# Kernel optimization log

Hardware: AMD Instinct MI355X
Metric: run time of the kernel (lower is better)

The kernel has to match this reference:

```python
import jax, jax.numpy as jnp
import numpy as np

G, N, F_IN, H, C = 128, 512, 128, 128, 10
LAMB = 1.0
NEG_SLOPE = 0.2
P_EDGE = 32.0 / N  # avg degree ~32


def setup_inputs() -> dict:
    key = jax.random.key(0)
    ks = jax.random.split(key, 12)
    x = jax.random.normal(ks[0], (G, N, F_IN), dtype=jnp.float32)
    # symmetric 0/1 adjacency without self loops (per-graph dense block)
    a = (jax.random.uniform(ks[1], (G, N, N)) < P_EDGE).astype(jnp.float32)
    adj = jnp.maximum(a, jnp.swapaxes(a, 1, 2)) * (1.0 - jnp.eye(N, dtype=jnp.float32))

    def lin(k, fi, fo):
        return (jax.random.normal(k, (fi, fo), dtype=jnp.float32) / np.float32(np.sqrt(fi)))

    return {
        "x": x, "adj": adj,
        "W1": lin(ks[2], F_IN, H), "b1": jnp.zeros((H,), jnp.float32),
        "W2": lin(ks[3], H, H), "b2": jnp.zeros((H,), jnp.float32),
        "W3": lin(ks[4], H, H), "b3": jnp.zeros((H,), jnp.float32),
        "att1_s": 0.1 * jax.random.normal(ks[5], (H,), dtype=jnp.float32),
        "att1_d": 0.1 * jax.random.normal(ks[6], (H,), dtype=jnp.float32),
        "att2_s": 0.1 * jax.random.normal(ks[7], (H,), dtype=jnp.float32),
        "att2_d": 0.1 * jax.random.normal(ks[8], (H,), dtype=jnp.float32),
        "Wl1": lin(ks[9], 2 * H, H), "bl1": jnp.zeros((H,), jnp.float32),
        "Wl2": lin(ks[10], H, H // 2), "bl2": jnp.zeros((H // 2,), jnp.float32),
        "Wl3": lin(ks[11], H // 2, C), "bl3": jnp.zeros((C,), jnp.float32),
    }


def gcn(x, adj, W, b):
    # GCNConv: D^{-1/2} (A + I) D^{-1/2} X W + b  (self-loop weight 1, edge weights in adj)
    deg = adj.sum(-1) + 1.0                              # [G, n]
    dinv = jax.lax.rsqrt(deg)
    xw = x @ W                                           # [G, n, H]
    agg = jnp.einsum('gij,gjf->gif', adj, dinv[..., None] * xw)
    return dinv[..., None] * agg + (dinv * dinv)[..., None] * xw + b


def info_score(x, adj):
    # HGP-SL node information score: row-wise L1 norm of (I - D^{-1} A) X
    deg = jnp.maximum(adj.sum(-1), 1.0)
    agg = jnp.einsum('gij,gjf->gif', adj, x) / deg[..., None]
    return jnp.sum(jnp.abs(x - agg), axis=-1)            # [G, n]


def hgpsl_pool(x, adj, att_s, att_d, k):
    # top-k node selection by information score, then structure learning:
    # dense (sample=False) path: e_ij = leaky_relu(att.[x_i||x_j]) + lamb*A_ij, softmax over j
    s = info_score(x, adj)
    _, idx = jax.lax.top_k(s, k)                         # [G, k]
    xk = jnp.take_along_axis(x, idx[..., None], axis=1)  # [G, k, H]
    g = jnp.arange(x.shape[0])[:, None, None]
    ak = adj[g, idx[:, :, None], idx[:, None, :]]        # induced adjacency [G, k, k]
    e = jax.nn.leaky_relu((xk @ att_s)[:, :, None] + (xk @ att_d)[:, None, :], NEG_SLOPE)
    attn = jax.nn.softmax(e + LAMB * ak, axis=-1)        # new learned edge weights
    return xk, attn


def readout(x):
    # gmp || gap over nodes
    return jnp.concatenate([x.max(axis=1), x.mean(axis=1)], axis=-1)


def reference(x, adj, W1, b1, W2, b2, W3, b3, att1_s, att1_d, att2_s, att2_d,
              Wl1, bl1, Wl2, bl2, Wl3, bl3):
    h = jax.nn.relu(gcn(x, adj, W1, b1))
    h, a1 = hgpsl_pool(h, adj, att1_s, att1_d, N // 2)
    x1 = readout(h)
    h = jax.nn.relu(gcn(h, a1, W2, b2))
    h, a2 = hgpsl_pool(h, a1, att2_s, att2_d, N // 4)
    x2 = readout(h)
    h = jax.nn.relu(gcn(h, a2, W3, b3))
    x3 = readout(h)
    z = jax.nn.relu(x1) + jax.nn.relu(x2) + jax.nn.relu(x3)
    z = jax.nn.relu(z @ Wl1 + bl1)
    z = jax.nn.relu(z @ Wl2 + bl2)
    return jax.nn.softmax(z @ Wl3 + bl3, axis=-1)
```

## Files before the change

### kernel.cpp

```cpp
#include <hip/hip_runtime.h>

#define Gg   128
#define N1   512
#define FH   128
#define K1   256
#define K2   128

typedef __bf16 bf16x8 __attribute__((ext_vector_type(8)));
typedef float  floatx4 __attribute__((ext_vector_type(4)));

__device__ inline float wredsum(float v) {
#pragma unroll
    for (int o = 32; o; o >>= 1) v += __shfl_xor(v, o, 64);
    return v;
}
__device__ inline float wredmax(float v) {
#pragma unroll
    for (int o = 32; o; o >>= 1) v = fmaxf(v, __shfl_xor(v, o, 64));
    return v;
}
__device__ inline unsigned short bf_rne(float x) {
    unsigned u = __float_as_uint(x);
    return (unsigned short)((u + 0x7fffu + ((u >> 16) & 1u)) >> 16);
}
__device__ __forceinline__ void gll16(const void* gsrc, void* lds) {
    __builtin_amdgcn_global_load_lds(
        (const __attribute__((address_space(1))) unsigned int*)gsrc,
        (__attribute__((address_space(3))) unsigned int*)lds, 16, 0, 0);
}

__global__ __launch_bounds__(256) void k_prep_gemm(const float* __restrict__ adj,
        unsigned short* __restrict__ adjbf,
        float* __restrict__ dinv_gcn, float* __restrict__ dinv_info,
        const float* __restrict__ A, const float* __restrict__ W, float* __restrict__ C) {
    __shared__ float Al[64][68];
    __shared__ float Wl[64][132];
    if (blockIdx.x < Gg * N1 / 64) {
        long long row0 = (long long)blockIdx.x * 64;
        int tid = threadIdx.x, tr = tid >> 4, tc = tid & 15;
        float acc[4][8] = {};
        for (int ch = 0; ch < 2; ++ch) {
            for (int p = tid; p < 1024; p += 256) {
                int r = p >> 4, c4 = p & 15;
                *(float4*)&Al[r][c4 * 4] = *(const float4*)(A + (row0 + r) * 128 + ch * 64 + c4 * 4);
            }
            for (int p = tid; p < 2048; p += 256) {
                int r = p >> 5, c4 = p & 31;
                *(float4*)&Wl[r][c4 * 4] = *(const float4*)(W + (ch * 64 + r) * 128 + c4 * 4);
            }
            __syncthreads();
            for (int k = 0; k < 64; ++k) {
                float4 w0 = *(const float4*)&Wl[k][tc * 8];
                float4 w1 = *(const float4*)&Wl[k][tc * 8 + 4];
                float w[8] = {w0.x, w0.y, w0.z, w0.w, w1.x, w1.y, w1.z, w1.w};
#pragma unroll
                for (int i = 0; i < 4; ++i) {
                    float a = Al[tr * 4 + i][k];
#pragma unroll
                    for (int j = 0; j < 8; ++j) acc[i][j] = fmaf(a, w[j], acc[i][j]);
                }
            }
            __syncthreads();
        }
#pragma unroll
        for (int i = 0; i < 4; ++i) {
            long long r = row0 + tr * 4 + i;
            *(float4*)(C + r * 128 + tc * 8)     = make_float4(acc[i][0], acc[i][1], acc[i][2], acc[i][3]);
            *(float4*)(C + r * 128 + tc * 8 + 4) = make_float4(acc[i][4], acc[i][5], acc[i][6], acc[i][7]);
        }
    } else {
        int wave = threadIdx.x >> 6, lane = threadIdx.x & 63;
        long long row = (long long)(blockIdx.x - Gg * N1 / 64) * 4 + wave;
        const float* ar = adj + row * N1;
        float s = 0.f;
        unsigned short ub[8] __attribute__((aligned(16)));
#pragma unroll
        for (int c = 0; c < 2; ++c) {
            float4 v = *(const float4*)(ar + lane * 8 + c * 4);
            s += (v.x + v.y) + (v.z + v.w);
            ub[c * 4 + 0] = (unsigned short)(__float_as_uint(v.x) >> 16);
            ub[c * 4 + 1] = (unsigned short)(__float_as_uint(v.y) >> 16);
            ub[c * 4 + 2] = (unsigned short)(__float_as_uint(v.z) >> 16);
            ub[c * 4 + 3] = (unsigned short)(__float_as_uint(v.w) >> 16);
        }
        *(uint4*)(adjbf + row * N1 + lane * 8) = *(const uint4*)ub;
        s = wredsum(s);
        if (lane == 0) {
            dinv_gcn[row]  = rsqrtf(s + 1.0f);
            dinv_info[row] = 1.0f / fmaxf(s, 1.0f);
        }
    }
}

__global__ __launch_bounds__(256) void k_tsplit(const float* __restrict__ feat,
        const float* __restrict__ rs,
        unsigned short* __restrict__ Thi, unsigned short* __restrict__ Tmid,
        unsigned short* __restrict__ Tlo) {
    __shared__ float tile[64 * 65];
    int b = blockIdx.x;
    int g = b >> 4, rb = (b >> 1) & 7, cb = b & 1;
    int t = threadIdx.x;
    {
        int r0 = t >> 4, c4 = t & 15;
#pragma unroll
        for (int i = 0; i < 4; ++i) {
            int r = r0 + i * 16;
            float4 v = *(const float4*)(feat + ((long long)g * 512 + rb * 64 + r) * 128 + cb * 64 + c4 * 4);
            if (rs) {
                float sc = rs[(long long)g * 512 + rb * 64 + r];
                v.x *= sc; v.y *= sc; v.z *= sc; v.w *= sc;
            }
            tile[r * 65 + c4 * 4 + 0] = v.x;
            tile[r * 65 + c4 * 4 + 1] = v.y;
            tile[r * 65 + c4 * 4 + 2] = v.z;
            tile[r * 65 + c4 * 4 + 3] = v.w;
        }
    }
    __syncthreads();
    int tf = t >> 2, chunk = t & 3;
    unsigned short hbuf[16] __attribute__((aligned(16)));
    unsigned short mbuf[16] __attribute__((aligned(16)));
    unsigned short lbuf[16] __attribute__((aligned(16)));
#pragma unroll
    for (int i = 0; i < 16; ++i) {
        int m = chunk * 16 + i;
        float v = tile[m * 65 + tf];
        unsigned short h = bf_rne(v);
        float fh = __uint_as_float((unsigned)h << 16);
        float r1 = v - fh;
        unsigned short md = bf_rne(r1);
        float fm = __uint_as_float((unsigned)md << 16);
        float r2 = r1 - fm;
        unsigned short lo = bf_rne(r2);
        hbuf[i] = h; mbuf[i] = md; lbuf[i] = lo;
    }
    int sxz = (tf >> 1) & 3;
    int c0 = (chunk & 1) * 2;
    int p0 = (c0 ^ sxz) * 8, p1 = ((c0 + 1) ^ sxz) * 8;
    long long obase = (long long)g * 65536 + (rb * 2 + (chunk >> 1)) * 4096
                    + (cb * 64 + tf) * 32;
    *(uint4*)(Thi + obase + p0)  = *(const uint4*)&hbuf[0];
    *(uint4*)(Thi + obase + p1)  = *(const uint4*)&hbuf[8];
    *(uint4*)(Tmid + obase + p0) = *(const uint4*)&mbuf[0];
    *(uint4*)(Tmid + obase + p1) = *(const uint4*)&mbuf[8];
    *(uint4*)(Tlo + obase + p0)  = *(const uint4*)&lbuf[0];
    *(uint4*)(Tlo + obase + p1)  = *(const uint4*)&lbuf[8];
}

template<int EPI>
__global__ __launch_bounds__(256) void k_aggmm(const unsigned short* __restrict__ adjbf,
        const unsigned short* __restrict__ Bhi, const unsigned short* __restrict__ Bmid,
        const unsigned short* __restrict__ Blo,
        const float* __restrict__ dvec, const float* __restrict__ hx,
        const float* __restrict__ bias, float* __restrict__ outH, float* __restrict__ outS) {
    __shared__ unsigned short Al[2][4096];
    __shared__ unsigned short Blin[2][3][4096];
    __shared__ float sred[2][128];
    int b = blockIdx.x;
    int g  = (b & 7) + ((b >> 5) << 3);
    int rb = (b >> 3) & 3;
    int tid = threadIdx.x;
    int w = tid >> 6, lane = tid & 63;
    int wm = w >> 1, wn = w & 1;
    int ln = lane & 15, quad = lane >> 4;
    int aoff = ((quad ^ ((lane >> 1) & 3)) << 4);
    floatx4 acc[4][4];
#pragma unroll
    for (int i = 0; i < 4; ++i)
#pragma unroll
        for (int j = 0; j < 4; ++j) { floatx4 z = {0.f, 0.f, 0.f, 0.f}; acc[i][j] = z; }

    const char* bsrc0 = (const char*)(Bhi  + (long long)g * 65536);
    const char* bsrc1 = (const char*)(Bmid + (long long)g * 65536);
    const char* bsrc2 = (const char*)(Blo  + (long long)g * 65536);
    int r1 = w * 32 + (lane >> 2);
    int c1 = (lane & 3) ^ ((r1 >> 1) & 3);
    int r2 = r1 + 16;
    int c2 = (lane & 3) ^ ((r2 >> 1) & 3);
    const unsigned short* abase = adjbf + ((long long)g * 512 + rb * 128) * 512;
    const unsigned short* asrc1 = abase + (long long)r1 * 512 + c1 * 8;
    const unsigned short* asrc2 = abase + (long long)r2 * 512 + c2 * 8;

#define STAGE(bi, kkv) do {                                                   \
        char* aldst = (char*)&Al[bi][0] + w * 2048;                           \
        gll16(asrc1 + (kkv), aldst);                                          \
        gll16(asrc2 + (kkv), aldst + 1024);                                   \
        long long soff = (long long)((kkv) >> 5) * 8192 + (w * 2048) + (lane << 4); \
        char* l0 = (char*)&Blin[bi][0][0] + w * 2048;                         \
        char* l1 = (char*)&Blin[bi][1][0] + w * 2048;                         \
        char* l2 = (char*)&Blin[bi][2][0] + w * 2048;                         \
        gll16(bsrc0 + soff,        l0);                                       \
        gll16(bsrc0 + soff + 1024, l0 + 1024);                                \
        gll16(bsrc1 + soff,        l1);                                       \
        gll16(bsrc1 + soff + 1024, l1 + 1024);                                \
        gll16(bsrc2 + soff,        l2);                                       \
        gll16(bsrc2 + soff + 1024, l2 + 1024);                                \
    } while (0)

    STAGE(0, 0);
    for (int kk = 0; kk < 512; kk += 32) {
        int cur = (kk >> 5) & 1;
        if (kk + 32 < 512) {
            STAGE(cur ^ 1, kk + 32);
            asm volatile("s_waitcnt vmcnt(8)" ::: "memory");
        } else {
            asm volatile("s_waitcnt vmcnt(0)" ::: "memory");
        }
        __builtin_amdgcn_sched_barrier(0);
        __builtin_amdgcn_s_barrier();
        bf16x8 af[4];
#pragma unroll
        for (int tm = 0; tm < 4; ++tm)
            af[tm] = *(const bf16x8*)((const char*)&Al[cur][0] + (wm * 64 + tm * 16 + ln) * 64 + aoff);
#pragma unroll
        for (int s = 0; s < 3; ++s) {
#pragma unroll
            for (int tn = 0; tn < 4; ++tn) {
                bf16x8 bfr = *(const bf16x8*)((const char*)&Blin[cur][s][0]
                                              + (wn * 64 + tn * 16 + ln) * 64 + aoff);
#pragma unroll
                for (int tm = 0; tm < 4; ++tm)
                    acc[tm][tn] = __builtin_amdgcn_mfma_f32_16x16x32_bf16(af[tm], bfr, acc[tm][tn], 0, 0, 0);
            }
        }
        __builtin_amdgcn_sched_barrier(0);
        __builtin_amdgcn_s_barrier();
    }
#undef STAGE
    long long rowbase = (long long)g * 512 + rb * 128;
    if (EPI == 0) {
#pragma unroll
        for (int tm = 0; tm < 4; ++tm)
#pragma unroll
        for (int r = 0; r < 4; ++r) {
            int ml = wm * 64 + tm * 16 + quad * 4 + r;
            long long grow = rowbase + ml;
            float di = dvec[grow];
#pragma unroll
            for (int tn = 0; tn < 4; ++tn) {
                int nc = wn * 64 + tn * 16 + ln;
                float hv = hx[grow * 128 + nc];
                float o = fmaxf(fmaf(di, acc[tm][tn][r] + di * hv, bias[nc]), 0.f);
                outH[grow * 128 + nc] = o;
            }
        }
    } else {
#pragma unroll
        for (int tm = 0; tm < 4; ++tm)
#pragma unroll
        for (int r = 0; r < 4; ++r) {
            int ml = wm * 64 + tm * 16 + quad * 4 + r;
            long long grow = rowbase + ml;
            float di = dvec[grow];
            float v = 0.f;
#pragma unroll
            for (int tn = 0; tn < 4; ++tn) {
                int nc = wn * 64 + tn * 16 + ln;
                float hv = hx[grow * 128 + nc];
                v += fabsf(hv - acc[tm][tn][r] * di);
            }
            v += __shfl_xor(v, 1); v += __shfl_xor(v, 2);
            v += __shfl_xor(v, 4); v += __shfl_xor(v, 8);
            if (ln == 0) sred[wn][ml] = v;
        }
        __syncthreads();
        if (tid < 128) outS[rowbase + tid] = sred[0][tid] + sred[1][tid];
    }
}

__global__ __launch_bounds__(256) void k_gemm_rw(const float* __restrict__ A,
        const float* __restrict__ W, float* __restrict__ C,
        const float* __restrict__ rs) {
    __shared__ float Al[64][68];
    __shared__ float Wl[64][132];
    long long row0 = (long long)blockIdx.x * 64;
    int tid = threadIdx.x, tr = tid >> 4, tc = tid & 15;
    float acc[4][8] = {};
    for (int ch = 0; ch < 2; ++ch) {
        for (int p = tid; p < 1024; p += 256) {
            int r = p >> 4, c4 = p & 15;
            *(float4*)&Al[r][c4 * 4] = *(const float4*)(A + (row0 + r) * 128 + ch * 64 + c4 * 4);
        }
        for (int p = tid; p < 2048; p += 256) {
            int r = p >> 5, c4 = p & 31;
            *(float4*)&Wl[r][c4 * 4] = *(const float4*)(W + (ch * 64 + r) * 128 + c4 * 4);
        }
        __syncthreads();
        for (int k = 0; k < 64; ++k) {
            float4 w0 = *(const float4*)&Wl[k][tc * 8];
            float4 w1 = *(const float4*)&Wl[k][tc * 8 + 4];
            float w[8] = {w0.x, w0.y, w0.z, w0.w, w1.x, w1.y, w1.z, w1.w};
#pragma unroll
            for (int i = 0; i < 4; ++i) {
                float a = Al[tr * 4 + i][k];
#pragma unroll
                for (int j = 0; j < 8; ++j) acc[i][j] = fmaf(a, w[j], acc[i][j]);
            }
        }
        __syncthreads();
    }
#pragma unroll
    for (int i = 0; i < 4; ++i) {
        long long r = row0 + tr * 4 + i;
        float sc = rs ? rs[r] : 1.0f;
        *(float4*)(C + r * 128 + tc * 8)     = make_float4(sc * acc[i][0], sc * acc[i][1], sc * acc[i][2], sc * acc[i][3]);
        *(float4*)(C + r * 128 + tc * 8 + 4) = make_float4(sc * acc[i][4], sc * acc[i][5], sc * acc[i][6], sc * acc[i][7]);
    }
}

template<int NT, int KSEL>
__global__ __launch_bounds__(256) void k_topk(const float* __restrict__ s, int* __restrict__ idx) {
    __shared__ unsigned long long keys[NT];
    int g = blockIdx.x;
    const float* sg = s + g * NT;
    for (int t = threadIdx.x; t < NT; t += 256) {
        unsigned int b = __float_as_uint(sg[t]);
        unsigned int ord = (b & 0x80000000u) ? ~b : (b | 0x80000000u);
        keys[t] = ((unsigned long long)(~ord) << 32) | (unsigned int)t;
    }
    __syncthreads();
    for (int k = 2; k <= NT; k <<= 1) {
        for (int j = k >> 1; j > 0; j >>= 1) {
            for (int i = threadIdx.x; i < NT; i += 256) {
                int l = i ^ j;
                if (l > i) {
                    bool dir = ((i & k) == 0);
                    unsigned long long a = keys[i], b2 = keys[l];
                    bool sw = dir ? (a > b2) : (a < b2);
                    if (sw) { keys[i] = b2; keys[l] = a; }
                }
            }
            __syncthreads();
        }
    }
    for (int t = threadIdx.x; t < KSEL; t += 256)
        idx[g * KSEL + t] = (int)(keys[t] & 0xffffffffu);
}

template<int KK>
__global__ __launch_bounds__(256) void k_gather(const float* __restrict__ h, int srcN,
        const int* __restrict__ idx, const float* __restrict__ atts, const float* __restrict__ attd,
        float* __restrict__ xk, float* __restrict__ as_, float* __restrict__ ad_) {
    int wave = threadIdx.x >> 6, lane = threadIdx.x & 63;
    int r = blockIdx.x * 4 + wave;
    int g = r / KK;
    int j = idx[r];
    float2 v = *(const float2*)(h + ((long long)g * srcN + j) * 128 + lane * 2);
    *(float2*)(xk + (long long)r * 128 + lane * 2) = v;
    float2 sv = *(const float2*)(atts + lane * 2);
    float2 dv = *(const float2*)(attd + lane * 2);
    float ps = v.x * sv.x + v.y * sv.y;
    float pd = v.x * dv.x + v.y * dv.y;
    ps = wredsum(ps); pd = wredsum(pd);
    if (lane == 0) { as_[r] = ps; ad_[r] = pd; }
}

template<int KK, int SRCN, bool BF16>
__global__ __launch_bounds__(256) void k_attnro(const void* __restrict__ adjSrc,
        const int* __restrict__ idx, const float* __restrict__ as_, const float* __restrict__ ad_,
        float* __restrict__ attn, float* __restrict__ dgo, float* __restrict__ dio,
        const float* __restrict__ xk, float* __restrict__ xo) {
    constexpr int E = KK / 64;
    constexpr int nAttn = Gg * KK / 4;
    __shared__ int   idxL[KK];
    __shared__ float adL[KK];
    __shared__ float rowL[4][SRCN];
    if ((int)blockIdx.x >= nAttn) {
        int g = blockIdx.x - nAttn, t = threadIdx.x;
        if (t < 128) {
            const float* p = xk + (long long)g * KK * 128 + t;
            float m = -1e30f, s = 0.f;
            for (int r = 0; r < KK; ++r) { float v = p[r * 128]; m = fmaxf(m, v); s += v; }
            xo[g * 256 + t] = m;
            xo[g * 256 + 128 + t] = s * (1.0f / KK);
        }
        return;
    }
    int bpg = KK / 4;
    int g = blockIdx.x / bpg;
    int wave = threadIdx.x >> 6, lane = threadIdx.x & 63;
    int i = (blockIdx.x % bpg) * 4 + wave;
    for (int t = threadIdx.x; t < KK; t += 256) { idxL[t] = idx[g * KK + t]; adL[t] = ad_[g * KK + t]; }
    __syncthreads();
    int ri = idxL[i];
    if (BF16) {
        const unsigned short* arow = (const unsigned short*)adjSrc + ((long long)g * SRCN + ri) * SRCN;
        for (int c = lane; c < SRCN; c += 64)
            rowL[wave][c] = __uint_as_float((unsigned)arow[c] << 16);
    } else {
        const float* arow = (const float*)adjSrc + ((long long)g * SRCN + ri) * SRCN;
        for (int c = lane; c < SRCN; c += 64) rowL[wave][c] = arow[c];
    }
    float asi = as_[g * KK + i];
    float vals[E];
    float m = -1e30f;
#pragma unroll
    for (int e = 0; e < E; ++e) {
        int j = e * 64 + lane;
        float x = asi + adL[j];
        x = (x >= 0.f) ? x : 0.2f * x;
        x += rowL[wave][idxL[j]];
        vals[e] = x; m = fmaxf(m, x);
    }
    m = wredmax(m);
    float S = 0.f;
#pragma unroll
    for (int e = 0; e < E; ++e) { vals[e] = expf(vals[e] - m); S += vals[e]; }
    S = wredsum(S);
    float inv = 1.f / S, rs = 0.f;
    float* orow = attn + ((long long)g * KK + i) * KK;
#pragma unroll
    for (int e = 0; e < E; ++e) { float p = vals[e] * inv; rs += p; orow[e * 64 + lane] = p; }
    rs = wredsum(rs);
    if (lane == 0) { dgo[g * KK + i] = rsqrtf(rs + 1.f); dio[g * KK + i] = 1.f / fmaxf(rs, 1.f); }
}

template<int KK, bool SCALEY, int EPI>
__global__ __launch_bounds__(256) void k_agg(const float* __restrict__ A, const float* __restrict__ Y,
        const float* __restrict__ dg, const float* __restrict__ di_,
        const float* __restrict__ bias, const float* __restrict__ hx,
        float* __restrict__ outH, float* __restrict__ outS) {
    __shared__ float Al[64][68];
    __shared__ float Yl[64][132];
    __shared__ float red[64][17];
    constexpr int RB = KK / 64;
    int g = blockIdx.x / RB;
    int rb = blockIdx.x % RB;
    const float* Ag = A + (long long)g * KK * KK;
    const float* Yg = Y + (long long)g * KK * 128;
    int tid = threadIdx.x, tr = tid >> 4, tc = tid & 15;
    float acc[4][8] = {};
    for (int ch = 0; ch < KK / 64; ++ch) {
        for (int p = tid; p < 1024; p += 256) {
            int r = p >> 4, c4 = p & 15;
            *(float4*)&Al[r][c4 * 4] = *(const float4*)(Ag + (rb * 64 + r) * KK + ch * 64 + c4 * 4);
        }
        for (int p = tid; p < 2048; p += 256) {
            int r = p >> 5, c4 = p & 31;
            float4 v = *(const float4*)(Yg + (ch * 64 + r) * 128 + c4 * 4);
            if (SCALEY) { float sc = dg[g * KK + ch * 64 + r]; v.x *= sc; v.y *= sc; v.z *= sc; v.w *= sc; }
            *(float4*)&Yl[r][c4 * 4] = v;
        }
        __syncthreads();
        for (int k = 0; k < 64; ++k) {
            float4 w0 = *(const float4*)&Yl[k][tc * 8];
            float4 w1 = *(const float4*)&Yl[k][tc * 8 + 4];
            float w[8] = {w0.x, w0.y, w0.z, w0.w, w1.x, w1.y, w1.z, w1.w};
#pragma unroll
            for (int i = 0; i < 4; ++i) {
                float a = Al[tr * 4 + i][k];
#pragma unroll
                for (int j = 0; j < 8; ++j) acc[i][j] = fmaf(a, w[j], acc[i][j]);
            }
        }
        __syncthreads();
    }
    int i0 = rb * 64 + tr * 4;
    if (EPI == 0) {
#pragma unroll
        for (int i = 0; i < 4; ++i) {
            long long gi = (long long)g * KK + i0 + i;
            float d = dg[gi], dd = d * d;
            float4 x0 = *(const float4*)(hx + gi * 128 + tc * 8);
            float4 x1 = *(const float4*)(hx + gi * 128 + tc * 8 + 4);
            float4 b0 = *(const float4*)(bias + tc * 8);
            float4 b1 = *(const float4*)(bias + tc * 8 + 4);
            float4 o0, o1;
            o0.x = fmaxf(fmaf(d, acc[i][0], fmaf(dd, x0.x, b0.x)), 0.f);
            o0.y = fmaxf(fmaf(d, acc[i][1], fmaf(dd, x0.y, b0.y)), 0.f);
            o0.z = fmaxf(fmaf(d, acc[i][2], fmaf(dd, x0.z, b0.z)), 0.f);
            o0.w = fmaxf(fmaf(d, acc[i][3], fmaf(dd, x0.w, b0.w)), 0.f);
            o1.x = fmaxf(fmaf(d, acc[i][4], fmaf(dd, x1.x, b1.x)), 0.f);
            o1.y = fmaxf(fmaf(d, acc[i][5], fmaf(dd, x1.y, b1.y)), 0.f);
            o1.z = fmaxf(fmaf(d, acc[i][6], fmaf(dd, x1.z, b1.z)), 0.f);
            o1.w = fmaxf(fmaf(d, acc[i][7], fmaf(dd, x1.w, b1.w)), 0.f);
            *(float4*)(outH + gi * 128 + tc * 8)     = o0;
            *(float4*)(outH + gi * 128 + tc * 8 + 4) = o1;
        }
    } else {
#pragma unroll
        for (int i = 0; i < 4; ++i) {
            long long gi = (long long)g * KK + i0 + i;
            float d = di_[gi];
            float4 x0 = *(const float4*)(hx + gi * 128 + tc * 8);
            float4 x1 = *(const float4*)(hx + gi * 128 + tc * 8 + 4);
            float p = fabsf(x0.x - acc[i][0] * d) + fabsf(x0.y - acc[i][1] * d)
                    + fabsf(x0.z - acc[i][2] * d) + fabsf(x0.w - acc[i][3] * d)
                    + fabsf(x1.x - acc[i][4] * d) + fabsf(x1.y - acc[i][5] * d)
                    + fabsf(x1.z - acc[i][6] * d) + fabsf(x1.w - acc[i][7] * d);
            red[tr * 4 + i][tc] = p;
        }
        __syncthreads();
        if (tid < 64) {
            float s = 0.f;
#pragma unroll
            for (int t = 0; t < 16; ++t) s += red[tid][t];
            outS[(long long)g * KK + rb * 64 + tid] = s;
        }
    }
}

__global__ __launch_bounds__(128) void k_mlp(const float* __restrict__ x1, const float* __restrict__ x2,
        const float* __restrict__ h3,
        const float* __restrict__ Wl1, const float* __restrict__ bl1,
        const float* __restrict__ Wl2, const float* __restrict__ bl2,
        const float* __restrict__ Wl3, const float* __restrict__ bl3,
        float* __restrict__ out) {
    __shared__ float z[256], z1[128], z2[64], lg[10];
    int g = blockIdx.x, t = threadIdx.x;
    {
        const float* p = h3 + (long long)g * K2 * 128 + t;
        float m = -1e30f, s = 0.f;
        for (int r = 0; r < K2; ++r) { float v = p[r * 128]; m = fmaxf(m, v); s += v; }
        float x3a = m, x3b = s * (1.0f / K2);
        z[t]       = fmaxf(x1[g * 256 + t], 0.f)       + fmaxf(x2[g * 256 + t], 0.f)       + fmaxf(x3a, 0.f);
        z[t + 128] = fmaxf(x1[g * 256 + 128 + t], 0.f) + fmaxf(x2[g * 256 + 128 + t], 0.f) + fmaxf(x3b, 0.f);
    }
    __syncthreads();
    {
        float acc = bl1[t];
        for (int k = 0; k < 256; ++k) acc = fmaf(z[k], Wl1[k * 128 + t], acc);
        z1[t] = fmaxf(acc, 0.f);
    }
    __syncthreads();
    if (t < 64) {
        float acc = bl2[t];
        for (int k = 0; k < 128; ++k) acc = fmaf(z1[k], Wl2[k * 64 + t], acc);
        z2[t] = fmaxf(acc, 0.f);
    }
    __syncthreads();
    if (t < 10) {
        float acc = bl3[t];
        for (int k = 0; k < 64; ++k) acc = fmaf(z2[k], Wl3[k * 10 + t], acc);
        lg[t] = acc;
    }
    __syncthreads();
    if (t == 0) {
        float m = -1e30f;
        for (int c = 0; c < 10; ++c) m = fmaxf(m, lg[c]);
        float S = 0.f;
        float e[10];
        for (int c = 0; c < 10; ++c) { e[c] = expf(lg[c] - m); S += e[c]; }
        float inv = 1.f / S;
        for (int c = 0; c < 10; ++c) out[g * 10 + c] = e[c] * inv;
    }
}

extern "C" void kernel_launch(void* const* d_in, const int* in_sizes, int n_in,
                              void* d_out, int out_size, void* d_ws, size_t ws_size,
                              hipStream_t stream) {
    const float* x     = (const float*)d_in[0];
    const float* adj   = (const float*)d_in[1];
    const float* W1    = (const float*)d_in[2];
    const float* b1    = (const float*)d_in[3];
    const float* W2    = (const float*)d_in[4];
    const float* b2    = (const float*)d_in[5];
    const float* W3    = (const float*)d_in[6];
    const float* b3    = (const float*)d_in[7];
    const float* att1s = (const float*)d_in[8];
    const float* att1d = (const float*)d_in[9];
    const float* att2s = (const float*)d_in[10];
    const float* att2d = (const float*)d_in[11];
    const float* Wl1   = (const float*)d_in[12];
    const float* bl1   = (const float*)d_in[13];
    const float* Wl2   = (const float*)d_in[14];
    const float* bl2   = (const float*)d_in[15];
    const float* Wl3   = (const float*)d_in[16];
    const float* bl3   = (const float*)d_in[17];
    float* out = (float*)d_out;

    char* ws = (char*)d_ws;
    unsigned short* Thi  = (unsigned short*)(ws + 0);
    unsigned short* Tmid = (unsigned short*)(ws + 16777216);
    unsigned short* Tlo  = (unsigned short*)(ws + 33554432);
    float* xk1 = (float*)(ws + 0);
    float* xw2 = (float*)(ws + 16777216);
    float* h2  = (float*)(ws + 33554432);
    float* xk2 = (float*)(ws + 16777216);
    float* a2  = (float*)(ws + 25165824);
    float* xw3 = (float*)(ws + 0);
    float* h3  = (float*)(ws + 8388608);
    float* dxw1 = (float*)(ws + 50331648);
    float* h1   = dxw1;
    float* a1   = dxw1;
    float* s1      = (float*)(ws + 83886080);
    int*   idx1    = (int*)  (ws + 84148224);
    float* as1     = (float*)(ws + 84279296);
    float* ad1     = (float*)(ws + 84410368);
    float* dinv_g1 = (float*)(ws + 84541440);
    float* dinv_i1 = (float*)(ws + 84803584);
    float* dinv_g2 = (float*)(ws + 85065728);
    float* dinv_i2 = (float*)(ws + 85196800);
    float* x1r     = (float*)(ws + 85327872);
    float* s2      = (float*)(ws + 85458944);
    int*   idx2    = (int*)  (ws + 85590016);
    float* as2     = (float*)(ws + 85655552);
    float* ad2     = (float*)(ws + 85721088);
    float* dinv_g3 = (float*)(ws + 85786624);
    float* dinv_i3 = (float*)(ws + 85852160);
    float* x2r     = (float*)(ws + 85917696);
    unsigned short* adjbf = (unsigned short*)(ws + 100663296);

    k_prep_gemm<<<Gg * N1 / 64 + Gg * N1 / 4, 256, 0, stream>>>(adj, adjbf, dinv_g1, dinv_i1, x, W1, dxw1);
    k_tsplit<<<Gg * 16, 256, 0, stream>>>(dxw1, dinv_g1, Thi, Tmid, Tlo);
    k_aggmm<0><<<Gg * 4, 256, 0, stream>>>(adjbf, Thi, Tmid, Tlo, dinv_g1, dxw1, b1, h1, nullptr);
    k_tsplit<<<Gg * 16, 256, 0, stream>>>(h1, nullptr, Thi, Tmid, Tlo);
    k_aggmm<1><<<Gg * 4, 256, 0, stream>>>(adjbf, Thi, Tmid, Tlo, dinv_i1, h1, nullptr, nullptr, s1);
    k_topk<N1, K1><<<Gg, 256, 0, stream>>>(s1, idx1);
    k_gather<K1><<<Gg * K1 / 4, 256, 0, stream>>>(h1, N1, idx1, att1s, att1d, xk1, as1, ad1);
    k_attnro<K1, N1, true><<<Gg * K1 / 4 + Gg, 256, 0, stream>>>(adjbf, idx1, as1, ad1, a1, dinv_g2, dinv_i2, xk1, x1r);

    k_gemm_rw<<<Gg * K1 / 64, 256, 0, stream>>>(xk1, W2, xw2, nullptr);
    k_agg<K1, true, 0><<<Gg * (K1 / 64), 256, 0, stream>>>(a1, xw2, dinv_g2, dinv_i2, b2, xw2, h2, nullptr);
    k_agg<K1, false, 1><<<Gg * (K1 / 64), 256, 0, stream>>>(a1, h2, dinv_g2, dinv_i2, b2, h2, nullptr, s2);
    k_topk<K1, K2><<<Gg, 256, 0, stream>>>(s2, idx2);
    k_gather<K2><<<Gg * K2 / 4, 256, 0, stream>>>(h2, K1, idx2, att2s, att2d, xk2, as2, ad2);
    k_attnro<K2, K1, false><<<Gg * K2 / 4 + Gg, 256, 0, stream>>>(a1, idx2, as2, ad2, a2, dinv_g3, dinv_i3, xk2, x2r);

    k_gemm_rw<<<Gg * K2 / 64, 256, 0, stream>>>(xk2, W3, xw3, nullptr);
    k_agg<K2, true, 0><<<Gg * (K2 / 64), 256, 0, stream>>>(a2, xw3, dinv_g3, dinv_i3, b3, xw3, h3, nullptr);

    k_mlp<<<Gg, 128, 0, stream>>>(x1r, x2r, h3, Wl1, bl1, Wl2, bl2, Wl3, bl3, out);
}
```

Before: 580.4 us.

## Reorder first GCN layer to aggregate inputs before applying W1 via split-bf16 MFMA

```diff
diff --git a/kernel.cpp b/kernel.cpp
--- a/kernel.cpp
+++ b/kernel.cpp
@@ -29,75 +29,57 @@
         (__attribute__((address_space(3))) unsigned int*)lds, 16, 0, 0);
 }
 
-__global__ __launch_bounds__(256) void k_prep_gemm(const float* __restrict__ adj,
+__global__ __launch_bounds__(256) void k_prep(const float* __restrict__ adj,
         unsigned short* __restrict__ adjbf,
-        float* __restrict__ dinv_gcn, float* __restrict__ dinv_info,
-        const float* __restrict__ A, const float* __restrict__ W, float* __restrict__ C) {
-    __shared__ float Al[64][68];
-    __shared__ float Wl[64][132];
-    if (blockIdx.x < Gg * N1 / 64) {
-        long long row0 = (long long)blockIdx.x * 64;
-        int tid = threadIdx.x, tr = tid >> 4, tc = tid & 15;
-        float acc[4][8] = {};
-        for (int ch = 0; ch < 2; ++ch) {
-            for (int p = tid; p < 1024; p += 256) {
-                int r = p >> 4, c4 = p & 15;
-                *(float4*)&Al[r][c4 * 4] = *(const float4*)(A + (row0 + r) * 128 + ch * 64 + c4 * 4);
-            }
-            for (int p = tid; p < 2048; p += 256) {
-                int r = p >> 5, c4 = p & 31;
-                *(float4*)&Wl[r][c4 * 4] = *(const float4*)(W + (ch * 64 + r) * 128 + c4 * 4);
-            }
-            __syncthreads();
-            for (int k = 0; k < 64; ++k) {
-                float4 w0 = *(const float4*)&Wl[k][tc * 8];
-                float4 w1 = *(const float4*)&Wl[k][tc * 8 + 4];
-                float w[8] = {w0.x, w0.y, w0.z, w0.w, w1.x, w1.y, w1.z, w1.w};
-#pragma unroll
-                for (int i = 0; i < 4; ++i) {
-                    float a = Al[tr * 4 + i][k];
-#pragma unroll
-                    for (int j = 0; j < 8; ++j) acc[i][j] = fmaf(a, w[j], acc[i][j]);
-                }
-            }
-            __syncthreads();
-        }
-#pragma unroll
-        for (int i = 0; i < 4; ++i) {
-            long long r = row0 + tr * 4 + i;
-            *(float4*)(C + r * 128 + tc * 8)     = make_float4(acc[i][0], acc[i][1], acc[i][2], acc[i][3]);
-            *(float4*)(C + r * 128 + tc * 8 + 4) = make_float4(acc[i][4], acc[i][5], acc[i][6], acc[i][7]);
-        }
-    } else {
-        int wave = threadIdx.x >> 6, lane = threadIdx.x & 63;
-        long long row = (long long)(blockIdx.x - Gg * N1 / 64) * 4 + wave;
-        const float* ar = adj + row * N1;
-        float s = 0.f;
-        unsigned short ub[8] __attribute__((aligned(16)));
-#pragma unroll
-        for (int c = 0; c < 2; ++c) {
-            float4 v = *(const float4*)(ar + lane * 8 + c * 4);
-            s += (v.x + v.y) + (v.z + v.w);
-            ub[c * 4 + 0] = (unsigned short)(__float_as_uint(v.x) >> 16);
-            ub[c * 4 + 1] = (unsigned short)(__float_as_uint(v.y) >> 16);
-            ub[c * 4 + 2] = (unsigned short)(__float_as_uint(v.z) >> 16);
-            ub[c * 4 + 3] = (unsigned short)(__float_as_uint(v.w) >> 16);
-        }
-        *(uint4*)(adjbf + row * N1 + lane * 8) = *(const uint4*)ub;
-        s = wredsum(s);
-        if (lane == 0) {
-            dinv_gcn[row]  = rsqrtf(s + 1.0f);
-            dinv_info[row] = 1.0f / fmaxf(s, 1.0f);
-        }
+        float* __restrict__ dinv_gcn, float* __restrict__ dinv_info) {
+    int wave = threadIdx.x >> 6, lane = threadIdx.x & 63;
+    long long row = (long long)blockIdx.x * 4 + wave;
+    const float* ar = adj + row * N1;
+    float s = 0.f;
+    unsigned short ub[8] __attribute__((aligned(16)));
+#pragma unroll
+    for (int c = 0; c < 2; ++c) {
+        float4 v = *(const float4*)(ar + lane * 8 + c * 4);
+        s += (v.x + v.y) + (v.z + v.w);
+        ub[c * 4 + 0] = (unsigned short)(__float_as_uint(v.x) >> 16);
+        ub[c * 4 + 1] = (unsigned short)(__float_as_uint(v.y) >> 16);
+        ub[c * 4 + 2] = (unsigned short)(__float_as_uint(v.z) >> 16);
+        ub[c * 4 + 3] = (unsigned short)(__float_as_uint(v.w) >> 16);
+    }
+    *(uint4*)(adjbf + row * N1 + lane * 8) = *(const uint4*)ub;
+    s = wredsum(s);
+    if (lane == 0) {
+        dinv_gcn[row]  = rsqrtf(s + 1.0f);
+        dinv_info[row] = 1.0f / fmaxf(s, 1.0f);
     }
 }
 
 __global__ __launch_bounds__(256) void k_tsplit(const float* __restrict__ feat,
         const float* __restrict__ rs,
         unsigned short* __restrict__ Thi, unsigned short* __restrict__ Tmid,
-        unsigned short* __restrict__ Tlo) {
+        unsigned short* __restrict__ Tlo,
+        const float* __restrict__ W1src,
+        unsigned short* __restrict__ WtH, unsigned short* __restrict__ WtM,
+        unsigned short* __restrict__ WtL) {
     __shared__ float tile[64 * 65];
     int b = blockIdx.x;
+    if (b == Gg * 16) {
+        for (int e = threadIdx.x; e < 16384; e += 256) {
+            int k = e >> 7, n = e & 127;
+            float v = W1src[k * 128 + n];
+            unsigned short h = bf_rne(v);
+            float fh = __uint_as_float((unsigned)h << 16);
+            float r1 = v - fh;
+            unsigned short md = bf_rne(r1);
+            float fm = __uint_as_float((unsigned)md << 16);
+            unsigned short lo = bf_rne(r1 - fm);
+            int ks = k >> 5, kc = k & 31;
+            int pos = ((((kc >> 3) ^ ((n >> 1) & 3)) << 3) | (kc & 7));
+            int o = ks * 4096 + n * 32 + pos;
+            WtH[o] = h; WtM[o] = md; WtL[o] = lo;
+        }
+        return;
+    }
     int g = b >> 4, rb = (b >> 1) & 7, cb = b & 1;
     int t = threadIdx.x;
     {
@@ -152,7 +134,9 @@
         const unsigned short* __restrict__ Bhi, const unsigned short* __restrict__ Bmid,
         const unsigned short* __restrict__ Blo,
         const float* __restrict__ dvec, const float* __restrict__ hx,
-        const float* __restrict__ bias, float* __restrict__ outH, float* __restrict__ outS) {
+        const float* __restrict__ bias, float* __restrict__ outH, float* __restrict__ outS,
+        unsigned short* __restrict__ zH, unsigned short* __restrict__ zM,
+        unsigned short* __restrict__ zL) {
     __shared__ unsigned short Al[2][4096];
     __shared__ unsigned short Blin[2][3][4096];
     __shared__ float sred[2][128];
@@ -244,7 +228,7 @@
                 outH[grow * 128 + nc] = o;
             }
         }
-    } else {
+    } else if (EPI == 1) {
 #pragma unroll
         for (int tm = 0; tm < 4; ++tm)
 #pragma unroll
@@ -265,6 +249,133 @@
         }
         __syncthreads();
         if (tid < 128) outS[rowbase + tid] = sred[0][tid] + sred[1][tid];
+    } else {
+#pragma unroll
+        for (int tm = 0; tm < 4; ++tm)
+#pragma unroll
+        for (int r = 0; r < 4; ++r) {
+            int ml = wm * 64 + tm * 16 + quad * 4 + r;
+            long long grow = rowbase + ml;
+            float di = dvec[grow];
+#pragma unroll
+            for (int tn = 0; tn < 4; ++tn) {
+                int nc = wn * 64 + tn * 16 + ln;
+                float xv = hx[grow * 128 + nc];
+                float v = acc[tm][tn][r] + di * xv;
+                unsigned short h = bf_rne(v);
+                float fh = __uint_as_float((unsigned)h << 16);
+                float rr = v - fh;
+                unsigned short md = bf_rne(rr);
+                float fm = __uint_as_float((unsigned)md << 16);
+                unsigned short lo = bf_rne(rr - fm);
+                zH[grow * 128 + nc] = h;
+                zM[grow * 128 + nc] = md;
+                zL[grow * 128 + nc] = lo;
+            }
+        }
+    }
+}
+
+__global__ __launch_bounds__(256) void k_h1mm(
+        const unsigned short* __restrict__ zH, const unsigned short* __restrict__ zM,
+        const unsigned short* __restrict__ zL,
+        const unsigned short* __restrict__ WtH, const unsigned short* __restrict__ WtM,
+        const unsigned short* __restrict__ WtL,
+        const float* __restrict__ dvec, const float* __restrict__ bias,
+        float* __restrict__ outH) {
+    __shared__ unsigned short As[2][3][4096];
+    __shared__ unsigned short Bs[2][3][4096];
+    int b = blockIdx.x;
+    long long row0 = (long long)b * 128;
+    int tid = threadIdx.x;
+    int w = tid >> 6, lane = tid & 63;
+    int wm = w >> 1, wn = w & 1;
+    int ln = lane & 15, quad = lane >> 4;
+    int aoff = ((quad ^ ((lane >> 1) & 3)) << 4);
+    floatx4 acc[4][4];
+#pragma unroll
+    for (int i = 0; i < 4; ++i)
+#pragma unroll
+        for (int j = 0; j < 4; ++j) { floatx4 z = {0.f, 0.f, 0.f, 0.f}; acc[i][j] = z; }
+
+    int r1 = w * 32 + (lane >> 2);
+    int c1 = (lane & 3) ^ ((r1 >> 1) & 3);
+    int r2 = r1 + 16;
+    int c2 = (lane & 3) ^ ((r2 >> 1) & 3);
+    const unsigned short* ah1 = zH + (row0 + r1) * 128 + c1 * 8;
+    const unsigned short* ah2 = zH + (row0 + r2) * 128 + c2 * 8;
+    const unsigned short* am1 = zM + (row0 + r1) * 128 + c1 * 8;
+    const unsigned short* am2 = zM + (row0 + r2) * 128 + c2 * 8;
+    const unsigned short* al1 = zL + (row0 + r1) * 128 + c1 * 8;
+    const unsigned short* al2 = zL + (row0 + r2) * 128 + c2 * 8;
+
+#define STAGEH(bi, kkv) do {                                                  \
+        char* ad0 = (char*)&As[bi][0][0] + w * 2048;                          \
+        char* ad1 = (char*)&As[bi][1][0] + w * 2048;                          \
+        char* ad2 = (char*)&As[bi][2][0] + w * 2048;                          \
+        gll16(ah1 + (kkv), ad0);  gll16(ah2 + (kkv), ad0 + 1024);             \
+        gll16(am1 + (kkv), ad1);  gll16(am2 + (kkv), ad1 + 1024);             \
+        gll16(al1 + (kkv), ad2);  gll16(al2 + (kkv), ad2 + 1024);             \
+        long long soff = (long long)((kkv) >> 5) * 8192 + (w * 2048) + (lane << 4); \
+        char* l0 = (char*)&Bs[bi][0][0] + w * 2048;                           \
+        char* l1 = (char*)&Bs[bi][1][0] + w * 2048;                           \
+        char* l2 = (char*)&Bs[bi][2][0] + w * 2048;                           \
+        gll16((const char*)WtH + soff,        l0);                            \
+        gll16((const char*)WtH + soff + 1024, l0 + 1024);                     \
+        gll16((const char*)WtM + soff,        l1);                            \
+        gll16((const char*)WtM + soff + 1024, l1 + 1024);                     \
+        gll16((const char*)WtL + soff,        l2);                            \
+        gll16((const char*)WtL + soff + 1024, l2 + 1024);                     \
+    } while (0)
+
+    STAGEH(0, 0);
+    for (int kk = 0; kk < 128; kk += 32) {
+        int cur = (kk >> 5) & 1;
+        if (kk + 32 < 128) {
+            STAGEH(cur ^ 1, kk + 32);
+            asm volatile("s_waitcnt vmcnt(12)" ::: "memory");
+        } else {
+            asm volatile("s_waitcnt vmcnt(0)" ::: "memory");
+        }
+        __builtin_amdgcn_sched_barrier(0);
+        __builtin_amdgcn_s_barrier();
+        bf16x8 af[3][4];
+#pragma unroll
+        for (int s = 0; s < 3; ++s)
+#pragma unroll
+        for (int tm = 0; tm < 4; ++tm)
+            af[s][tm] = *(const bf16x8*)((const char*)&As[cur][s][0] + (wm * 64 + tm * 16 + ln) * 64 + aoff);
+#pragma unroll
+        for (int tn = 0; tn < 4; ++tn) {
+            bf16x8 bh = *(const bf16x8*)((const char*)&Bs[cur][0][0] + (wn * 64 + tn * 16 + ln) * 64 + aoff);
+            bf16x8 bm = *(const bf16x8*)((const char*)&Bs[cur][1][0] + (wn * 64 + tn * 16 + ln) * 64 + aoff);
+            bf16x8 bl = *(const bf16x8*)((const char*)&Bs[cur][2][0] + (wn * 64 + tn * 16 + ln) * 64 + aoff);
+#pragma unroll
+            for (int tm = 0; tm < 4; ++tm) {
+                acc[tm][tn] = __builtin_amdgcn_mfma_f32_16x16x32_bf16(af[0][tm], bh, acc[tm][tn], 0, 0, 0);
+                acc[tm][tn] = __builtin_amdgcn_mfma_f32_16x16x32_bf16(af[0][tm], bm, acc[tm][tn], 0, 0, 0);
+                acc[tm][tn] = __builtin_amdgcn_mfma_f32_16x16x32_bf16(af[1][tm], bh, acc[tm][tn], 0, 0, 0);
+                acc[tm][tn] = __builtin_amdgcn_mfma_f32_16x16x32_bf16(af[0][tm], bl, acc[tm][tn], 0, 0, 0);
+                acc[tm][tn] = __builtin_amdgcn_mfma_f32_16x16x32_bf16(af[1][tm], bm, acc[tm][tn], 0, 0, 0);
+                acc[tm][tn] = __builtin_amdgcn_mfma_f32_16x16x32_bf16(af[2][tm], bh, acc[tm][tn], 0, 0, 0);
+            }
+        }
+        __builtin_amdgcn_sched_barrier(0);
+        __builtin_amdgcn_s_barrier();
+    }
+#undef STAGEH
+#pragma unroll
+    for (int tm = 0; tm < 4; ++tm)
+#pragma unroll
+    for (int r = 0; r < 4; ++r) {
+        int ml = wm * 64 + tm * 16 + quad * 4 + r;
+        long long grow = row0 + ml;
+        float di = dvec[grow];
+#pragma unroll
+        for (int tn = 0; tn < 4; ++tn) {
+            int nc = wn * 64 + tn * 16 + ln;
+            outH[grow * 128 + nc] = fmaxf(fmaf(di, acc[tm][tn][r], bias[nc]), 0.f);
+        }
     }
 }
 
@@ -580,9 +691,8 @@
     float* a2  = (float*)(ws + 25165824);
     float* xw3 = (float*)(ws + 0);
     float* h3  = (float*)(ws + 8388608);
-    float* dxw1 = (float*)(ws + 50331648);
-    float* h1   = dxw1;
-    float* a1   = dxw1;
+    float* h1  = (float*)(ws + 50331648);
+    float* a1  = h1;
     float* s1      = (float*)(ws + 83886080);
     int*   idx1    = (int*)  (ws + 84148224);
     float* as1     = (float*)(ws + 84279296);
@@ -600,12 +710,21 @@
     float* dinv_i3 = (float*)(ws + 85852160);
     float* x2r     = (float*)(ws + 85917696);
     unsigned short* adjbf = (unsigned short*)(ws + 100663296);
-
-    k_prep_gemm<<<Gg * N1 / 64 + Gg * N1 / 4, 256, 0, stream>>>(adj, adjbf, dinv_g1, dinv_i1, x, W1, dxw1);
-    k_tsplit<<<Gg * 16, 256, 0, stream>>>(dxw1, dinv_g1, Thi, Tmid, Tlo);
-    k_aggmm<0><<<Gg * 4, 256, 0, stream>>>(adjbf, Thi, Tmid, Tlo, dinv_g1, dxw1, b1, h1, nullptr);
-    k_tsplit<<<Gg * 16, 256, 0, stream>>>(h1, nullptr, Thi, Tmid, Tlo);
-    k_aggmm<1><<<Gg * 4, 256, 0, stream>>>(adjbf, Thi, Tmid, Tlo, dinv_i1, h1, nullptr, nullptr, s1);
+    unsigned short* zH  = (unsigned short*)(ws + 268435456);
+    unsigned short* zM  = (unsigned short*)(ws + 285212672);
+    unsigned short* zL  = (unsigned short*)(ws + 301989888);
+    unsigned short* WtH = (unsigned short*)(ws + 335544320);
+    unsigned short* WtM = (unsigned short*)(ws + 335577088);
+    unsigned short* WtL = (unsigned short*)(ws + 335609856);
+
+    k_prep<<<Gg * N1 / 4, 256, 0, stream>>>(adj, adjbf, dinv_g1, dinv_i1);
+    k_tsplit<<<Gg * 16 + 1, 256, 0, stream>>>(x, dinv_g1, Thi, Tmid, Tlo, W1, WtH, WtM, WtL);
+    k_aggmm<2><<<Gg * 4, 256, 0, stream>>>(adjbf, Thi, Tmid, Tlo, dinv_g1, x, nullptr,
+                                           nullptr, nullptr, zH, zM, zL);
+    k_h1mm<<<Gg * 4, 256, 0, stream>>>(zH, zM, zL, WtH, WtM, WtL, dinv_g1, b1, h1);
+    k_tsplit<<<Gg * 16, 256, 0, stream>>>(h1, nullptr, Thi, Tmid, Tlo, nullptr, nullptr, nullptr, nullptr);
+    k_aggmm<1><<<Gg * 4, 256, 0, stream>>>(adjbf, Thi, Tmid, Tlo, dinv_i1, h1, nullptr,
+                                           nullptr, s1, nullptr, nullptr, nullptr);
     k_topk<N1, K1><<<Gg, 256, 0, stream>>>(s1, idx1);
     k_gather<K1><<<Gg * K1 / 4, 256, 0, stream>>>(h1, N1, idx1, att1s, att1d, xk1, as1, ad1);
     k_attnro<K1, N1, true><<<Gg * K1 / 4 + Gg, 256, 0, stream>>>(adjbf, idx1, as1, ad1, a1, dinv_g2, dinv_i2, xk1, x1r);
```

Result: slower. 615.0 us (+6.0%).
